# Kernel tuning notes

Hardware: AMD Instinct MI355X
Metric: run time of the kernel (lower is better)

The kernel has to match this reference:

```python
import jax, jax.numpy as jnp
import numpy as np


def setup_inputs() -> dict:
    key = jax.random.key(0)
    k1, k2, k3 = jax.random.split(key, 3)
    B, N, M, S = 2, 8192, 32768, 4096
    pred = jax.random.normal(k1, (B, N, 3), dtype=jnp.float32)
    target = jax.random.normal(k2, (B, M, 3), dtype=jnp.float32)
    # stands in for torch.randperm(N)[:S]; duplicates don't change the math shape-wise
    idx = jax.random.randint(k3, (S,), 0, N, dtype=jnp.int64)
    return {"pred": pred, "target": target, "idx": idx}


def reference(pred, target, idx):
    # pred: (B, N, 3), target: (B, M, 3), idx: (S,)
    pred_s = pred[:, idx, :]                       # (B, S, 3) -- sampled points
    x2 = jnp.sum(pred_s * pred_s, axis=-1)         # (B, S)
    y2 = jnp.sum(target * target, axis=-1)         # (B, M)
    xy = jnp.einsum("bsd,bmd->bsm", pred_s, target)  # (B, S, M)
    d2 = x2[:, :, None] + y2[:, None, :] - 2.0 * xy
    dist = jnp.sqrt(jnp.maximum(d2, 0.0))          # (B, S, M)
    min_dist = jnp.min(dist, axis=2)               # (B, S)
    return jnp.mean(min_dist)
```

## Files before the change

### kernel.cpp

```cpp
#include <hip/hip_runtime.h>
#include <math.h>

typedef float vf2 __attribute__((ext_vector_type(2)));
typedef float vf4 __attribute__((ext_vector_type(4)));

constexpr int B = 2;
constexpr int N = 8192;
constexpr int M = 32768;
constexpr int S = 4096;
constexpr int QTOT = B * S;
constexpr int R = 16;
constexpr int WT = 64 * R;
constexpr int TCH = M / WT;
constexpr int QG = S / 64;
constexpr int WAVES = B * TCH * QG;
constexpr int BLOCKS = WAVES / 4;

#define DECLP(j) vf2 T0_##j, T1_##j, T2_##j, TY_##j;

#define LOADQUAD(r, pA, pB)                                               \
  {                                                                       \
    vf4 u0 = gt[192 * (r) + 3 * lane];                                    \
    vf4 u1 = gt[192 * (r) + 3 * lane + 1];                                \
    vf4 u2 = gt[192 * (r) + 3 * lane + 2];                                \
    T0_##pA = vf2{u0.x, u0.w};                                            \
    T1_##pA = vf2{u0.y, u1.x};                                            \
    T2_##pA = vf2{u0.z, u1.y};                                            \
    TY_##pA = vf2{fmaf(u0.x, u0.x, fmaf(u0.y, u0.y, u0.z * u0.z)),        \
                  fmaf(u0.w, u0.w, fmaf(u1.x, u1.x, u1.y * u1.y))};       \
    T0_##pB = vf2{u1.z, u2.y};                                            \
    T1_##pB = vf2{u1.w, u2.z};                                            \
    T2_##pB = vf2{u2.x, u2.w};                                            \
    TY_##pB = vf2{fmaf(u1.z, u1.z, fmaf(u1.w, u1.w, u2.x * u2.x)),        \
                  fmaf(u2.y, u2.y, fmaf(u2.z, u2.z, u2.w * u2.w))};       \
  }

#define PAIRC(j, acc)                                                    \
  {                                                                      \
    vf2 s = __builtin_elementwise_fma(Q0, T0_##j, TY_##j);               \
    s = __builtin_elementwise_fma(Q1, T1_##j, s);                        \
    s = __builtin_elementwise_fma(Q2, T2_##j, s);                        \
    acc = fminf(fminf(s.x, s.y), acc);                   \
  }

__global__ __launch_bounds__(256, 4) void chamfer_main(
    const float* __restrict__ pred, const float* __restrict__ target,
    const int* __restrict__ idx, unsigned* __restrict__ wsmin) {
  __shared__ vf4 qv[64];
  const int lane = threadIdx.x & 63;
  const int w = blockIdx.x * 4 + (threadIdx.x >> 6);
  const int b = w >> 11;
  const int rem = w & 2047;
  const int tch = rem & (TCH - 1);
  const int qg = rem >> 5;

  if (threadIdx.x < 64) {
    int s = qg * 64 + threadIdx.x;
    int i = idx[s];
    const float* p = pred + ((size_t)b * N + (size_t)i) * 3;
    float x = p[0], y = p[1], z = p[2];
    qv[threadIdx.x] =
        vf4{-2.0f * x, -2.0f * y, -2.0f * z, fmaf(x, x, fmaf(y, y, z * z))};
  }

  const float* tb = target + ((size_t)b * M + (size_t)tch * WT) * 3;
  const vf4* gt = (const vf4*)tb;
  DECLP(0) DECLP(1) DECLP(2) DECLP(3) DECLP(4) DECLP(5) DECLP(6) DECLP(7)
  LOADQUAD(0, 0, 1) LOADQUAD(1, 2, 3) LOADQUAD(2, 4, 5) LOADQUAD(3, 6, 7)
  __syncthreads();

  const vf4 qh = qv[lane];
  const int rot = ((lane + 1) & 63) * 4;
  float mm = INFINITY;
  int qoff = lane;
  vf4 qc = qh;

#pragma unroll 1
  for (int step = 0; step < 64; ++step) {
    const int qn = (qoff + 1) & 63;
    vf4 nq = qv[qn];
    const vf2 Q0 = vf2{qc.x, qc.x};
    const vf2 Q1 = vf2{qc.y, qc.y};
    const vf2 Q2 = vf2{qc.z, qc.z};
    float m0 = INFINITY, m1 = INFINITY;
    PAIRC(0, m0) PAIRC(1, m1) PAIRC(2, m0) PAIRC(3, m1)
    PAIRC(4, m0) PAIRC(5, m1) PAIRC(6, m0) PAIRC(7, m1)
    mm = fminf(mm, fminf(m0, m1));
    mm = __int_as_float(__builtin_amdgcn_ds_bpermute(rot, __float_as_int(mm)));
    qc = nq;
    qoff = qn;
  }
  const int q = b * S + qg * 64 + lane;
  atomicMin(&wsmin[q], __float_as_uint(fmaxf(qh.w + mm, 0.0f)));
}

__global__ __launch_bounds__(1024) void chamfer_finish(
    const unsigned* __restrict__ wsmin, float* __restrict__ out) {
  __shared__ float red[16];
  const uint4* wm = (const uint4*)wsmin;
  float sum = 0.0f;
#pragma unroll
  for (int i = 0; i < QTOT / 4096; ++i) {
    uint4 v = wm[threadIdx.x + i * 1024];
    sum += sqrtf(__uint_as_float(v.x)) + sqrtf(__uint_as_float(v.y)) +
           sqrtf(__uint_as_float(v.z)) + sqrtf(__uint_as_float(v.w));
  }
#pragma unroll
  for (int off = 32; off > 0; off >>= 1)
    sum += __shfl_down(sum, off, 64);
  int wv = threadIdx.x >> 6;
  if ((threadIdx.x & 63) == 0) red[wv] = sum;
  __syncthreads();
  if (threadIdx.x == 0) {
    float t = 0.0f;
#pragma unroll
    for (int i = 0; i < 16; ++i) t += red[i];
    out[0] = t / (float)QTOT;
  }
}

extern "C" void kernel_launch(void* const* d_in, const int* in_sizes, int n_in,
                              void* d_out, int out_size, void* d_ws, size_t ws_size,
                              hipStream_t stream) {
  const float* pred = (const float*)d_in[0];
  const float* target = (const float*)d_in[1];
  const int* idx = (const int*)d_in[2];
  unsigned* wsmin = (unsigned*)d_ws;

  hipMemsetAsync(wsmin, 0xFF, QTOT * sizeof(unsigned), stream);
  chamfer_main<<<BLOCKS, 256, 0, stream>>>(pred, target, idx, wsmin);
  chamfer_finish<<<1, 1024, 0, stream>>>(wsmin, (float*)d_out);
}
```

Before: 82.68 us.

## Replace global atomicMin with block-level LDS reduction and per-chunk partial buffer

Each block's four waves cover four consecutive target chunks for the same 64 queries. Their per-query minima are now combined in shared memory and written as plain stores into a query-by-chunk-group buffer, instead of each wave issuing a global atomicMin. The finish kernel reads the eight partials per query and takes their minimum before the sqrt and sum. This removes the memset launch and the atomic contention, at the cost of a block-wide barrier at the end of the main kernel and a larger partial buffer to read back.

```diff
diff --git a/kernel.cpp b/kernel.cpp
--- a/kernel.cpp
+++ b/kernel.cpp
@@ -12,6 +12,7 @@
 constexpr int R = 16;
 constexpr int WT = 64 * R;
 constexpr int TCH = M / WT;
+constexpr int TG = TCH / 4;
 constexpr int QG = S / 64;
 constexpr int WAVES = B * TCH * QG;
 constexpr int BLOCKS = WAVES / 4;
@@ -45,8 +46,9 @@
 
 __global__ __launch_bounds__(256, 4) void chamfer_main(
     const float* __restrict__ pred, const float* __restrict__ target,
-    const int* __restrict__ idx, unsigned* __restrict__ wsmin) {
+    const int* __restrict__ idx, float* __restrict__ wsmin) {
   __shared__ vf4 qv[64];
+  __shared__ float cmb[4][64];
   const int lane = threadIdx.x & 63;
   const int w = blockIdx.x * 4 + (threadIdx.x >> 6);
   const int b = w >> 11;
@@ -90,20 +92,29 @@
     qc = nq;
     qoff = qn;
   }
-  const int q = b * S + qg * 64 + lane;
-  atomicMin(&wsmin[q], __float_as_uint(fmaxf(qh.w + mm, 0.0f)));
+  cmb[threadIdx.x >> 6][lane] = fmaxf(qh.w + mm, 0.0f);
+  __syncthreads();
+  if (threadIdx.x < 64) {
+    float v = fminf(fminf(cmb[0][threadIdx.x], cmb[1][threadIdx.x]),
+                    fminf(cmb[2][threadIdx.x], cmb[3][threadIdx.x]));
+    const int q = b * S + qg * 64 + threadIdx.x;
+    wsmin[q * TG + (tch >> 2)] = v;
+  }
 }
 
 __global__ __launch_bounds__(1024) void chamfer_finish(
-    const unsigned* __restrict__ wsmin, float* __restrict__ out) {
+    const float* __restrict__ wsmin, float* __restrict__ out) {
   __shared__ float red[16];
-  const uint4* wm = (const uint4*)wsmin;
+  const vf4* wm = (const vf4*)wsmin;
   float sum = 0.0f;
 #pragma unroll
-  for (int i = 0; i < QTOT / 4096; ++i) {
-    uint4 v = wm[threadIdx.x + i * 1024];
-    sum += sqrtf(__uint_as_float(v.x)) + sqrtf(__uint_as_float(v.y)) +
-           sqrtf(__uint_as_float(v.z)) + sqrtf(__uint_as_float(v.w));
+  for (int i = 0; i < QTOT / 1024; ++i) {
+    int q = threadIdx.x + i * 1024;
+    vf4 a = wm[2 * q];
+    vf4 c = wm[2 * q + 1];
+    float m = fminf(fminf(fminf(a.x, a.y), fminf(a.z, a.w)),
+                    fminf(fminf(c.x, c.y), fminf(c.z, c.w)));
+    sum += sqrtf(m);
   }
 #pragma unroll
   for (int off = 32; off > 0; off >>= 1)
@@ -125,9 +136,8 @@
   const float* pred = (const float*)d_in[0];
   const float* target = (const float*)d_in[1];
   const int* idx = (const int*)d_in[2];
-  unsigned* wsmin = (unsigned*)d_ws;
+  float* wsmin = (float*)d_ws;
 
-  hipMemsetAsync(wsmin, 0xFF, QTOT * sizeof(unsigned), stream);
   chamfer_main<<<BLOCKS, 256, 0, stream>>>(pred, target, idx, wsmin);
   chamfer_finish<<<1, 1024, 0, stream>>>(wsmin, (float*)d_out);
 }
```

Measured after the change: 84.99 us. 2.8% more time.
